# Performance work log

Hardware: AMD Instinct MI355X
Metric: run time of the kernel (lower is better)

Reference implementation:

```python
import jax, jax.numpy as jnp
import numpy as np
import math

WP, WF = 10, 10      # past/future window
EPS = 1e-8           # torch cosine_similarity eps
CLIP = 1.0 - 1e-6    # keep arccos (and its grad) finite
MAXN = 110           # hard-coded alpha width in the module


def setup_inputs() -> dict:
    key = jax.random.key(0)
    k1, k2, k3, k4, k5, k6 = jax.random.split(key, 6)
    B, L, G, N, D = 32, 110, 512, 40, 300
    node_features = jax.random.normal(k1, (B, L, G), jnp.float32)
    knowledge = jax.random.normal(k2, (B, L, N, D), jnp.float32)
    anew = jax.random.uniform(k3, (B, L, N), jnp.float32)
    var_sem = 2.0 / (G + G)
    var_con = 2.0 / (D + D)
    weight_sem = jax.random.normal(k4, (G, G), jnp.float32) * var_sem
    weight_con = jax.random.normal(k5, (D, D), jnp.float32) * var_con
    text_len = jax.random.randint(k6, (B,), 55, L + 1, jnp.int32)
    return dict(node_features=node_features, knowledge=knowledge, anew=anew,
                weight_sem=weight_sem, weight_con=weight_con, text_len=text_len)


def reference(node_features, knowledge, anew, weight_sem, weight_con, text_len):
    B, L, G = node_features.shape
    N = knowledge.shape[2]
    dt = node_features.dtype

    # window + validity mask, replaces per-(i,j) python slicing: [B, j, k]
    j = jnp.arange(L)[:, None]
    k = jnp.arange(L)[None, :]
    cur = text_len[:, None, None]
    mask = (k >= j - WP) & (k <= j + WF)
    mask = mask[None] & (k[None, :, :] <= cur - 1) & (j[None, :, :] < cur)
    fmask = mask.astype(dt)

    # ---- semantic branch: score = 1 - acos(cos_sim(f_j, W_sem f_k))/pi, windowed softmax
    att_sem = jnp.einsum('st,blt->bls', weight_sem, node_features)      # [B,L,G]
    num = jnp.einsum('bjg,bkg->bjk', node_features, att_sem)
    nf = jnp.maximum(jnp.linalg.norm(node_features, axis=-1), EPS)      # [B,L]
    na = jnp.maximum(jnp.linalg.norm(att_sem, axis=-1), EPS)            # [B,L]
    cos = num / (nf[:, :, None] * na[:, None, :])
    score = 1.0 - jnp.arccos(jnp.clip(cos, -CLIP, CLIP)) / math.pi
    neg = jnp.finfo(dt).min
    s = jnp.where(mask, score, neg)
    s = s - jnp.max(s, axis=-1, keepdims=True)
    e = jnp.exp(s) * fmask
    alphas_sem = e / jnp.maximum(jnp.sum(e, axis=-1, keepdims=True), EPS)  # [B,L,L]

    # ---- affinity transform of anew: v -> (||[v, v/2] - [0.5, 0]|| - 0.06467)/0.607468
    anew_aff = (jnp.sqrt((anew - 0.5) ** 2 + (0.5 * anew) ** 2) - 0.06467) / 0.607468

    # ---- contextual branch: windowed sum_n |cos_sim(aff_feat_{k,n}, knowledge_{j,n})|
    att_con = jnp.einsum('blns,st->blnt', knowledge, weight_con)        # [B,L,N,D]
    aff_feat = att_con * anew_aff[..., None]                            # [B,L,N,D]
    num_c = jnp.einsum('bknd,bjnd->bjkn', aff_feat, knowledge)          # [B,j,k,N]
    n_f = jnp.maximum(jnp.linalg.norm(aff_feat, axis=-1), EPS)          # [B,k,N]
    n_k = jnp.maximum(jnp.linalg.norm(knowledge, axis=-1), EPS)         # [B,j,N]
    cos_c = num_c / (n_f[:, None, :, :] * n_k[:, :, None, :])
    alphas_con = 10.0 * jnp.sum(jnp.abs(cos_c), axis=-1) * fmask        # [B,j,k]

    out = 0.5 * alphas_sem + 0.5 * alphas_con                           # [B,L,L]
    if L < MAXN:  # module hard-codes width 110
        out = jnp.pad(out, ((0, 0), (0, 0), (0, MAXN - L)))
    return out
```

## Files before the change

### kernel.cpp

```cpp
#include <hip/hip_runtime.h>
#include <hip/hip_bf16.h>
#include <math.h>

constexpr int Bb   = 32;
constexpr int Ls   = 110;
constexpr int Gs   = 512;
constexpr int Ns   = 40;
constexpr int Ds   = 300;
constexpr int WPc  = 10;
constexpr int WFc  = 10;
constexpr int MAXNc = 110;
constexpr float EPSf  = 1e-8f;
constexpr float CLIPf = 1.0f - 1e-6f;
constexpr int BL = Bb * Ls;
constexpr int Mrows = BL * Ns;

typedef __attribute__((ext_vector_type(8))) short short8_t;
typedef __attribute__((ext_vector_type(4))) short short4_t;
typedef __attribute__((ext_vector_type(4))) float floatx4;

__device__ __forceinline__ unsigned short bf16r(float f) {
  unsigned u = __float_as_uint(f);
  u += 0x7fffu + ((u >> 16) & 1u);
  return (unsigned short)(u >> 16);
}

__device__ __forceinline__ unsigned pkbf(float lo, float hi) {
  unsigned a = __float_as_uint(lo), b = __float_as_uint(hi);
  a += 0x7fffu + ((a >> 16) & 1u);
  b += 0x7fffu + ((b >> 16) & 1u);
  return (a >> 16) | (b & 0xffff0000u);
}

__device__ __forceinline__ short8_t cvt8(const float4 v0, const float4 v1) {
  union { short8_t s; unsigned u[4]; } p;
  p.u[0] = pkbf(v0.x, v0.y);
  p.u[1] = pkbf(v0.z, v0.w);
  p.u[2] = pkbf(v1.x, v1.y);
  p.u[3] = pkbf(v1.z, v1.w);
  return p.s;
}

__global__ __launch_bounds__(256) void transpose_wsem(const float* __restrict__ w,
                                                      float* __restrict__ wt) {
  __shared__ float tile[32][33];
  const int bx = blockIdx.x * 32;
  const int by = blockIdx.y * 32;
  const int tx = threadIdx.x;
  const int ty = threadIdx.y;
#pragma unroll
  for (int r = ty; r < 32; r += 8)
    tile[r][tx] = w[(by + r) * Gs + (bx + tx)];
  __syncthreads();
#pragma unroll
  for (int r = ty; r < 32; r += 8)
    wt[(bx + r) * Gs + (by + tx)] = tile[tx][r];
}

__global__ __launch_bounds__(256) void wct_prep(const float* __restrict__ wc,
                                                short* __restrict__ wct) {
  __shared__ float tile[32][33];
  const int t0 = blockIdx.x * 32;
  const int s0 = blockIdx.y * 32;
  const int tx = threadIdx.x, ty = threadIdx.y;
#pragma unroll
  for (int r = ty; r < 32; r += 8) {
    const int s = s0 + r, t = t0 + tx;
    tile[r][tx] = (s < Ds && t < Ds) ? wc[s * Ds + t] : 0.f;
  }
  __syncthreads();
#pragma unroll
  for (int r = ty; r < 32; r += 8) {
    const int t = t0 + r, s = s0 + tx;
    wct[t * 320 + s] = (short)bf16r(tile[tx][r]);
  }
}

__global__ __launch_bounds__(512) void sem_gemm(const float* __restrict__ nf,
                                                const float* __restrict__ wt,
                                                float* __restrict__ att_sem,
                                                float* __restrict__ na_arr) {
  const int bl0 = blockIdx.x * 8;
  const int s = threadIdx.x;
  const float* __restrict__ x0 = nf + (size_t)bl0 * Gs;
  float acc[8];
#pragma unroll
  for (int r = 0; r < 8; ++r) acc[r] = 0.f;
#pragma unroll 4
  for (int t = 0; t < Gs; ++t) {
    const float wv = wt[t * Gs + s];
#pragma unroll
    for (int r = 0; r < 8; ++r) acc[r] = fmaf(wv, x0[r * Gs + t], acc[r]);
  }
#pragma unroll
  for (int r = 0; r < 8; ++r) att_sem[(size_t)(bl0 + r) * Gs + s] = acc[r];

  __shared__ float partial[8][8];
  const int wave = s >> 6, lane = s & 63;
#pragma unroll
  for (int r = 0; r < 8; ++r) {
    float v = acc[r] * acc[r];
#pragma unroll
    for (int off = 32; off > 0; off >>= 1) v += __shfl_xor(v, off);
    if (lane == 0) partial[r][wave] = v;
  }
  __syncthreads();
  if (s < 8) {
    float sum = 0.f;
#pragma unroll
    for (int w2 = 0; w2 < 8; ++w2) sum += partial[s][w2];
    na_arr[bl0 + s] = fmaxf(sqrtf(sum), EPSf);
  }
}

__global__ __launch_bounds__(256) void sem_attn(const float* __restrict__ nf,
                                                const float* __restrict__ att_sem,
                                                const float* __restrict__ na_arr,
                                                const int* __restrict__ tlen,
                                                float* __restrict__ out) {
  const int blk = blockIdx.x;
  const int b = blk / Ls, j = blk % Ls;
  const int len = tlen[b];
  float* __restrict__ orow = out + (size_t)(b * Ls + j) * MAXNc;
  if (j >= len) {
    for (int k = threadIdx.x; k < MAXNc; k += 256) orow[k] = 0.f;
    return;
  }
  const int k0 = max(j - WPc, 0);
  const int k1 = min(j + WFc, len - 1);
  const int nk = k1 - k0 + 1;

  __shared__ float xs[Gs];
  __shared__ float sc[21];
  __shared__ float red[4];

  const float* __restrict__ x = nf + (size_t)(b * Ls + j) * Gs;
  float ss = 0.f;
  for (int t = threadIdx.x; t < Gs; t += 256) {
    const float v = x[t];
    xs[t] = v;
    ss += v * v;
  }
  const int wave = threadIdx.x >> 6, lane = threadIdx.x & 63;
#pragma unroll
  for (int off = 32; off > 0; off >>= 1) ss += __shfl_xor(ss, off);
  if (lane == 0) red[wave] = ss;
  __syncthreads();
  const float nfn = fmaxf(sqrtf(red[0] + red[1] + red[2] + red[3]), EPSf);

  for (int i = wave; i < nk; i += 4) {
    const int k = k0 + i;
    const float* __restrict__ as = att_sem + (size_t)(b * Ls + k) * Gs;
    float d = 0.f;
#pragma unroll
    for (int t = lane; t < Gs; t += 64) d = fmaf(xs[t], as[t], d);
#pragma unroll
    for (int off = 32; off > 0; off >>= 1) d += __shfl_xor(d, off);
    if (lane == 0) {
      float cs = d / (nfn * na_arr[b * Ls + k]);
      cs = fminf(fmaxf(cs, -CLIPf), CLIPf);
      sc[i] = 1.0f - acosf(cs) * (float)(1.0 / M_PI);
    }
  }
  __syncthreads();
  if (threadIdx.x == 0) {
    float m = -1e30f;
    for (int i = 0; i < nk; ++i) m = fmaxf(m, sc[i]);
    red[0] = m;
  }
  __syncthreads();
  const float m = red[0];
  if ((int)threadIdx.x < nk) sc[threadIdx.x] = expf(sc[threadIdx.x] - m);
  __syncthreads();
  if (threadIdx.x == 0) {
    float s = 0.f;
    for (int i = 0; i < nk; ++i) s += sc[i];
    red[1] = 1.0f / fmaxf(s, EPSf);
  }
  __syncthreads();
  const float inv = red[1];
  for (int k = threadIdx.x; k < MAXNc; k += 256) {
    float v = 0.f;
    if (k >= k0 && k <= k1) v = 0.5f * sc[k - k0] * inv;
    orow[k] = v;
  }
}

__global__ __launch_bounds__(256) void con_gemm_mfma(const float* __restrict__ kn,
                                                     const short* __restrict__ wct,
                                                     const float* __restrict__ anew,
                                                     const int* __restrict__ tlen,
                                                     unsigned short* __restrict__ ybar) {
  const int row0 = blockIdx.x * 64;
  {
    const int bl0 = row0 / Ns, bl1 = (row0 + 63) / Ns;
    bool alive = false;
    for (int bl = bl0; bl <= bl1; ++bl)
      if ((bl % Ls) < tlen[bl / Ls]) alive = true;
    if (!alive) return;
  }

  __shared__ float rowss[64][4];
  __shared__ float scl[64];

  const int tid = threadIdx.x;
  const int wave = tid >> 6, lane = tid & 63;
  const int quad = lane >> 4, l16 = lane & 15;

  floatx4 acc[4][5];
#pragma unroll
  for (int mt = 0; mt < 4; ++mt)
#pragma unroll
    for (int i = 0; i < 5; ++i) acc[mt][i] = (floatx4){0.f, 0.f, 0.f, 0.f};

  const float* arow[4];
#pragma unroll
  for (int mt = 0; mt < 4; ++mt)
    arow[mt] = kn + (size_t)(row0 + mt * 16 + l16) * Ds;

  const short* brow[5];
#pragma unroll
  for (int i = 0; i < 5; ++i)
    brow[i] = wct + (wave * 80 + i * 16 + l16) * 320 + quad * 8;

  for (int c = 0; c < 9; ++c) {
    const int d0 = c * 32 + quad * 8;
    short8_t bfrag[5];
#pragma unroll
    for (int i = 0; i < 5; ++i)
      bfrag[i] = *reinterpret_cast<const short8_t*>(brow[i] + c * 32);
#pragma unroll
    for (int mt = 0; mt < 4; ++mt) {
      const float4 v0 = *reinterpret_cast<const float4*>(arow[mt] + d0);
      const float4 v1 = *reinterpret_cast<const float4*>(arow[mt] + d0 + 4);
      const short8_t afrag = cvt8(v0, v1);
#pragma unroll
      for (int i = 0; i < 5; ++i)
        acc[mt][i] = __builtin_amdgcn_mfma_f32_16x16x32_bf16(afrag, bfrag[i], acc[mt][i], 0, 0, 0);
    }
  }

  {
    const int d0 = 288 + quad * 8;
    short8_t bfrag[5];
#pragma unroll
    for (int i = 0; i < 5; ++i)
      bfrag[i] = *reinterpret_cast<const short8_t*>(brow[i] + 288);
#pragma unroll
    for (int mt = 0; mt < 4; ++mt) {
      float4 v0 = make_float4(0.f, 0.f, 0.f, 0.f);
      float4 v1 = make_float4(0.f, 0.f, 0.f, 0.f);
      if (quad == 0) {
        v0 = *reinterpret_cast<const float4*>(arow[mt] + d0);
        v1 = *reinterpret_cast<const float4*>(arow[mt] + d0 + 4);
      } else if (quad == 1) {
        v0 = *reinterpret_cast<const float4*>(arow[mt] + d0);
      }
      const short8_t afrag = cvt8(v0, v1);
#pragma unroll
      for (int i = 0; i < 5; ++i)
        acc[mt][i] = __builtin_amdgcn_mfma_f32_16x16x32_bf16(afrag, bfrag[i], acc[mt][i], 0, 0, 0);
    }
  }

#pragma unroll
  for (int mt = 0; mt < 4; ++mt) {
#pragma unroll
    for (int r = 0; r < 4; ++r) {
      float p = 0.f;
#pragma unroll
      for (int i = 0; i < 5; ++i) {
        const float y = acc[mt][i][r];
        p = fmaf(y, y, p);
      }
      p += __shfl_xor(p, 1);
      p += __shfl_xor(p, 2);
      p += __shfl_xor(p, 4);
      p += __shfl_xor(p, 8);
      if (l16 == 0) rowss[mt * 16 + quad * 4 + r][wave] = p;
    }
  }
  __syncthreads();
  if (tid < 64) {
    const float ss = rowss[tid][0] + rowss[tid][1] + rowss[tid][2] + rowss[tid][3];
    const float a = anew[row0 + tid];
    const float aff = (sqrtf((a - 0.5f) * (a - 0.5f) + 0.25f * a * a) - 0.06467f) *
                      (1.0f / 0.607468f);
    scl[tid] = aff / fmaxf(aff * sqrtf(ss), EPSf);
  }
  __syncthreads();

#pragma unroll
  for (int mt = 0; mt < 4; ++mt) {
#pragma unroll
    for (int i = 0; i < 5; ++i) {
      const int col = wave * 80 + i * 16 + l16;
      if (col < Ds) {
#pragma unroll
        for (int r = 0; r < 4; ++r) {
          const int row = mt * 16 + quad * 4 + r;
          ybar[(size_t)(row0 + row) * Ds + col] = bf16r(acc[mt][i][r] * scl[row]);
        }
      }
    }
  }
}

__global__ __launch_bounds__(512) void con_attn_mfma(const float* __restrict__ kn,
                                                     const unsigned short* __restrict__ ybar,
                                                     const int* __restrict__ tlen,
                                                     float* __restrict__ out) {
  const int b = blockIdx.x / 7;
  const int jt = blockIdx.x % 7;
  const int j0 = jt * 16;
  const int len = tlen[b];
  if (j0 >= len) return;
  const int kbase = min(max(j0 - WPc, 0), Ls - 48);

  const int tid = threadIdx.x;
  const int wave = tid >> 6, lane = tid & 63;
  const int quad = lane >> 4, l16 = lane & 15;

  __shared__ float red[8][768];

  const int jj = min(j0 + l16, Ls - 1);
  const size_t blj = (size_t)(b * Ls + jj);

  float outacc[3][4];
#pragma unroll
  for (int t = 0; t < 3; ++t)
#pragma unroll
    for (int r = 0; r < 4; ++r) outacc[t][r] = 0.f;

  const unsigned short* yrow[3];
#pragma unroll
  for (int t = 0; t < 3; ++t) {
    const int k = kbase + t * 16 + l16;
    yrow[t] = ybar + ((size_t)(b * Ls + k) * Ns) * Ds;
  }

  for (int ni = 0; ni < 5; ++ni) {
    const int n = wave + ni * 8;
    const float* __restrict__ arow = kn + (blj * Ns + n) * Ds;

    floatx4 S[3];
#pragma unroll
    for (int t = 0; t < 3; ++t) S[t] = (floatx4){0.f, 0.f, 0.f, 0.f};
    float ssq = 0.f;

#pragma unroll
    for (int c = 0; c < 10; ++c) {
      const int d0 = c * 32 + quad * 8;
      float av[8];
      if (c < 9) {
        const float4 v0 = *reinterpret_cast<const float4*>(arow + d0);
        const float4 v1 = *reinterpret_cast<const float4*>(arow + d0 + 4);
        av[0] = v0.x; av[1] = v0.y; av[2] = v0.z; av[3] = v0.w;
        av[4] = v1.x; av[5] = v1.y; av[6] = v1.z; av[7] = v1.w;
      } else {
        if (quad == 0) {
          const float4 v0 = *reinterpret_cast<const float4*>(arow + d0);
          const float4 v1 = *reinterpret_cast<const float4*>(arow + d0 + 4);
          av[0] = v0.x; av[1] = v0.y; av[2] = v0.z; av[3] = v0.w;
          av[4] = v1.x; av[5] = v1.y; av[6] = v1.z; av[7] = v1.w;
        } else if (quad == 1) {
          const float4 v0 = *reinterpret_cast<const float4*>(arow + d0);
          av[0] = v0.x; av[1] = v0.y; av[2] = v0.z; av[3] = v0.w;
          av[4] = av[5] = av[6] = av[7] = 0.f;
        } else {
#pragma unroll
          for (int e = 0; e < 8; ++e) av[e] = 0.f;
        }
      }
      short8_t afrag;
#pragma unroll
      for (int e = 0; e < 8; ++e) {
        ssq = fmaf(av[e], av[e], ssq);
        afrag[e] = (short)bf16r(av[e]);
      }
#pragma unroll
      for (int t = 0; t < 3; ++t) {
        const unsigned short* yr = yrow[t] + (size_t)n * Ds;
        short8_t bfrag;
        if (c < 9) {
          const short4_t u0 = *reinterpret_cast<const short4_t*>(yr + d0);
          const short4_t u1 = *reinterpret_cast<const short4_t*>(yr + d0 + 4);
          bfrag[0] = u0.x; bfrag[1] = u0.y; bfrag[2] = u0.z; bfrag[3] = u0.w;
          bfrag[4] = u1.x; bfrag[5] = u1.y; bfrag[6] = u1.z; bfrag[7] = u1.w;
        } else {
          if (quad == 0) {
            const short4_t u0 = *reinterpret_cast<const short4_t*>(yr + d0);
            const short4_t u1 = *reinterpret_cast<const short4_t*>(yr + d0 + 4);
            bfrag[0] = u0.x; bfrag[1] = u0.y; bfrag[2] = u0.z; bfrag[3] = u0.w;
            bfrag[4] = u1.x; bfrag[5] = u1.y; bfrag[6] = u1.z; bfrag[7] = u1.w;
          } else if (quad == 1) {
            const short4_t u0 = *reinterpret_cast<const short4_t*>(yr + d0);
            bfrag[0] = u0.x; bfrag[1] = u0.y; bfrag[2] = u0.z; bfrag[3] = u0.w;
            bfrag[4] = bfrag[5] = bfrag[6] = bfrag[7] = 0;
          } else {
#pragma unroll
            for (int e = 0; e < 8; ++e) bfrag[e] = 0;
          }
        }
        S[t] = __builtin_amdgcn_mfma_f32_16x16x32_bf16(afrag, bfrag, S[t], 0, 0, 0);
      }
    }

    ssq += __shfl_xor(ssq, 16);
    ssq += __shfl_xor(ssq, 32);
    const float kinv = 1.0f / fmaxf(sqrtf(ssq), EPSf);

#pragma unroll
    for (int r = 0; r < 4; ++r) {
      const float kv = __shfl(kinv, quad * 4 + r);
#pragma unroll
      for (int t = 0; t < 3; ++t)
        outacc[t][r] = fmaf(kv, fabsf(S[t][r]), outacc[t][r]);
    }
  }

#pragma unroll
  for (int t = 0; t < 3; ++t)
#pragma unroll
    for (int r = 0; r < 4; ++r)
      red[wave][(quad * 4 + r) * 48 + t * 16 + l16] = outacc[t][r];
  __syncthreads();

  for (int idx = tid; idx < 768; idx += 512) {
    float s = 0.f;
#pragma unroll
    for (int w = 0; w < 8; ++w) s += red[w][idx];
    const int j = j0 + idx / 48;
    const int k = kbase + idx % 48;
    if (j < len && k < len && k >= j - WPc && k <= j + WFc)
      out[(size_t)(b * Ls + j) * MAXNc + k] += 5.0f * s;
  }
}

extern "C" void kernel_launch(void* const* d_in, const int* in_sizes, int n_in,
                              void* d_out, int out_size, void* d_ws, size_t ws_size,
                              hipStream_t stream) {
  const float* nf   = (const float*)d_in[0];
  const float* kn   = (const float*)d_in[1];
  const float* anew = (const float*)d_in[2];
  const float* wsem = (const float*)d_in[3];
  const float* wcon = (const float*)d_in[4];
  const int*   tlen = (const int*)d_in[5];
  float* out = (float*)d_out;

  float* att_sem = (float*)d_ws;
  float* na_arr  = att_sem + (size_t)BL * Gs;
  float* wt      = na_arr + BL;
  short* wct     = (short*)(wt + (size_t)Gs * Gs);
  unsigned short* ybar = (unsigned short*)(wct + 320 * 320);

  transpose_wsem<<<dim3(16, 16), dim3(32, 8), 0, stream>>>(wsem, wt);
  wct_prep<<<dim3(10, 10), dim3(32, 8), 0, stream>>>(wcon, wct);
  sem_gemm<<<BL / 8, 512, 0, stream>>>(nf, wt, att_sem, na_arr);
  sem_attn<<<BL, 256, 0, stream>>>(nf, att_sem, na_arr, tlen, out);
  con_gemm_mfma<<<Mrows / 64, 256, 0, stream>>>(kn, wct, anew, tlen, ybar);
  con_attn_mfma<<<Bb * 7, 512, 0, stream>>>(kn, ybar, tlen, out);
}
```

Before: 541.7 us.

## Split contextual GEMM over output columns, stage weights in LDS, defer row scaling

The contextual GEMM now runs on a 2D grid: each block computes 64 rows by 80 output columns, with one 16-row tile per wave. The block's slice of the bf16 weight is staged once in padded shared memory, and the fp32 knowledge rows are prefetched through a rotating 3-deep register pipeline. Row sums of squares are accumulated across column blocks with global atomics into a memset buffer, so ybar is stored unscaled. The attention kernel then applies the anew affinity scaling and norm per (k,n) itself. The aim is more parallelism and lower register pressure. The cost is that each A row is read four times, plus atomics, an extra memset, and extra per-iteration loads in the attention kernel.

Result: faster. 513.2 us (-5.2%).

```diff
diff --git a/kernel.cpp b/kernel.cpp
--- a/kernel.cpp
+++ b/kernel.cpp
@@ -14,6 +14,7 @@
 constexpr float CLIPf = 1.0f - 1e-6f;
 constexpr int BL = Bb * Ls;
 constexpr int Mrows = BL * Ns;
+constexpr int BPITCH = 328;
 
 typedef __attribute__((ext_vector_type(8))) short short8_t;
 typedef __attribute__((ext_vector_type(4))) short short4_t;
@@ -188,9 +189,9 @@
 
 __global__ __launch_bounds__(256) void con_gemm_mfma(const float* __restrict__ kn,
                                                      const short* __restrict__ wct,
-                                                     const float* __restrict__ anew,
                                                      const int* __restrict__ tlen,
-                                                     unsigned short* __restrict__ ybar) {
+                                                     unsigned short* __restrict__ ybar,
+                                                     float* __restrict__ rowss) {
   const int row0 = blockIdx.x * 64;
   {
     const int bl0 = row0 / Ns, bl1 = (row0 + 63) / Ns;
@@ -199,108 +200,89 @@
       if ((bl % Ls) < tlen[bl / Ls]) alive = true;
     if (!alive) return;
   }
-
-  __shared__ float rowss[64][4];
-  __shared__ float scl[64];
+  const int n0 = blockIdx.y * 80;
+
+  __shared__ short Bl[80 * BPITCH];
 
   const int tid = threadIdx.x;
   const int wave = tid >> 6, lane = tid & 63;
   const int quad = lane >> 4, l16 = lane & 15;
 
-  floatx4 acc[4][5];
-#pragma unroll
-  for (int mt = 0; mt < 4; ++mt)
-#pragma unroll
-    for (int i = 0; i < 5; ++i) acc[mt][i] = (floatx4){0.f, 0.f, 0.f, 0.f};
-
-  const float* arow[4];
-#pragma unroll
-  for (int mt = 0; mt < 4; ++mt)
-    arow[mt] = kn + (size_t)(row0 + mt * 16 + l16) * Ds;
-
-  const short* brow[5];
-#pragma unroll
-  for (int i = 0; i < 5; ++i)
-    brow[i] = wct + (wave * 80 + i * 16 + l16) * 320 + quad * 8;
-
-  for (int c = 0; c < 9; ++c) {
-    const int d0 = c * 32 + quad * 8;
-    short8_t bfrag[5];
-#pragma unroll
-    for (int i = 0; i < 5; ++i)
-      bfrag[i] = *reinterpret_cast<const short8_t*>(brow[i] + c * 32);
-#pragma unroll
-    for (int mt = 0; mt < 4; ++mt) {
-      const float4 v0 = *reinterpret_cast<const float4*>(arow[mt] + d0);
-      const float4 v1 = *reinterpret_cast<const float4*>(arow[mt] + d0 + 4);
-      const short8_t afrag = cvt8(v0, v1);
-#pragma unroll
-      for (int i = 0; i < 5; ++i)
-        acc[mt][i] = __builtin_amdgcn_mfma_f32_16x16x32_bf16(afrag, bfrag[i], acc[mt][i], 0, 0, 0);
-    }
-  }
-
-  {
-    const int d0 = 288 + quad * 8;
-    short8_t bfrag[5];
-#pragma unroll
-    for (int i = 0; i < 5; ++i)
-      bfrag[i] = *reinterpret_cast<const short8_t*>(brow[i] + 288);
-#pragma unroll
-    for (int mt = 0; mt < 4; ++mt) {
-      float4 v0 = make_float4(0.f, 0.f, 0.f, 0.f);
-      float4 v1 = make_float4(0.f, 0.f, 0.f, 0.f);
-      if (quad == 0) {
-        v0 = *reinterpret_cast<const float4*>(arow[mt] + d0);
-        v1 = *reinterpret_cast<const float4*>(arow[mt] + d0 + 4);
-      } else if (quad == 1) {
-        v0 = *reinterpret_cast<const float4*>(arow[mt] + d0);
+  for (int s = tid; s < 80 * 40; s += 256) {
+    const int nl = s / 40, slot = s % 40;
+    *reinterpret_cast<short8_t*>(&Bl[nl * BPITCH + slot * 8]) =
+        *reinterpret_cast<const short8_t*>(wct + (n0 + nl) * 320 + slot * 8);
+  }
+
+  const float* __restrict__ arow = kn + (size_t)(row0 + wave * 16 + l16) * Ds;
+
+  floatx4 acc[5];
+#pragma unroll
+  for (int i = 0; i < 5; ++i) acc[i] = (floatx4){0.f, 0.f, 0.f, 0.f};
+
+  float4 A0[3], A1[3];
+#pragma unroll
+  for (int p = 0; p < 2; ++p) {
+    const int d0 = p * 32 + quad * 8;
+    A0[p] = *reinterpret_cast<const float4*>(arow + d0);
+    A1[p] = *reinterpret_cast<const float4*>(arow + d0 + 4);
+  }
+  __syncthreads();
+
+#pragma unroll
+  for (int c = 0; c < 10; ++c) {
+    if (c < 8) {
+      const int pc = c + 2;
+      const int d0 = pc * 32 + quad * 8;
+      if (pc < 9) {
+        A0[pc % 3] = *reinterpret_cast<const float4*>(arow + d0);
+        A1[pc % 3] = *reinterpret_cast<const float4*>(arow + d0 + 4);
+      } else {
+        float4 v0 = make_float4(0.f, 0.f, 0.f, 0.f);
+        float4 v1 = make_float4(0.f, 0.f, 0.f, 0.f);
+        if (quad == 0) {
+          v0 = *reinterpret_cast<const float4*>(arow + d0);
+          v1 = *reinterpret_cast<const float4*>(arow + d0 + 4);
+        } else if (quad == 1) {
+          v0 = *reinterpret_cast<const float4*>(arow + d0);
+        }
+        A0[pc % 3] = v0;
+        A1[pc % 3] = v1;
       }
-      const short8_t afrag = cvt8(v0, v1);
-#pragma unroll
-      for (int i = 0; i < 5; ++i)
-        acc[mt][i] = __builtin_amdgcn_mfma_f32_16x16x32_bf16(afrag, bfrag[i], acc[mt][i], 0, 0, 0);
-    }
-  }
-
-#pragma unroll
-  for (int mt = 0; mt < 4; ++mt) {
-#pragma unroll
-    for (int r = 0; r < 4; ++r) {
-      float p = 0.f;
-#pragma unroll
-      for (int i = 0; i < 5; ++i) {
-        const float y = acc[mt][i][r];
-        p = fmaf(y, y, p);
-      }
-      p += __shfl_xor(p, 1);
-      p += __shfl_xor(p, 2);
-      p += __shfl_xor(p, 4);
-      p += __shfl_xor(p, 8);
-      if (l16 == 0) rowss[mt * 16 + quad * 4 + r][wave] = p;
-    }
-  }
-  __syncthreads();
-  if (tid < 64) {
-    const float ss = rowss[tid][0] + rowss[tid][1] + rowss[tid][2] + rowss[tid][3];
-    const float a = anew[row0 + tid];
-    const float aff = (sqrtf((a - 0.5f) * (a - 0.5f) + 0.25f * a * a) - 0.06467f) *
-                      (1.0f / 0.607468f);
-    scl[tid] = aff / fmaxf(aff * sqrtf(ss), EPSf);
-  }
-  __syncthreads();
-
-#pragma unroll
-  for (int mt = 0; mt < 4; ++mt) {
+    }
+    const short8_t afrag = cvt8(A0[c % 3], A1[c % 3]);
 #pragma unroll
     for (int i = 0; i < 5; ++i) {
-      const int col = wave * 80 + i * 16 + l16;
-      if (col < Ds) {
-#pragma unroll
-        for (int r = 0; r < 4; ++r) {
-          const int row = mt * 16 + quad * 4 + r;
-          ybar[(size_t)(row0 + row) * Ds + col] = bf16r(acc[mt][i][r] * scl[row]);
-        }
+      const short8_t bfrag = *reinterpret_cast<const short8_t*>(
+          &Bl[(i * 16 + l16) * BPITCH + c * 32 + quad * 8]);
+      acc[i] = __builtin_amdgcn_mfma_f32_16x16x32_bf16(afrag, bfrag, acc[i], 0, 0, 0);
+    }
+  }
+
+#pragma unroll
+  for (int r = 0; r < 4; ++r) {
+    float p = 0.f;
+#pragma unroll
+    for (int i = 0; i < 5; ++i) {
+      const float y = acc[i][r];
+      p = fmaf(y, y, p);
+    }
+    p += __shfl_xor(p, 1);
+    p += __shfl_xor(p, 2);
+    p += __shfl_xor(p, 4);
+    p += __shfl_xor(p, 8);
+    if (l16 == 0)
+      atomicAdd(&rowss[row0 + wave * 16 + quad * 4 + r], p);
+  }
+
+#pragma unroll
+  for (int i = 0; i < 5; ++i) {
+    const int col = n0 + i * 16 + l16;
+    if (col < Ds) {
+#pragma unroll
+      for (int r = 0; r < 4; ++r) {
+        const int row = row0 + wave * 16 + quad * 4 + r;
+        ybar[(size_t)row * Ds + col] = bf16r(acc[i][r]);
       }
     }
   }
@@ -308,6 +290,8 @@
 
 __global__ __launch_bounds__(512) void con_attn_mfma(const float* __restrict__ kn,
                                                      const unsigned short* __restrict__ ybar,
+                                                     const float* __restrict__ rowss,
+                                                     const float* __restrict__ anew,
                                                      const int* __restrict__ tlen,
                                                      float* __restrict__ out) {
   const int b = blockIdx.x / 7;
@@ -333,15 +317,28 @@
     for (int r = 0; r < 4; ++r) outacc[t][r] = 0.f;
 
   const unsigned short* yrow[3];
+  int krow_m[3];
 #pragma unroll
   for (int t = 0; t < 3; ++t) {
     const int k = kbase + t * 16 + l16;
     yrow[t] = ybar + ((size_t)(b * Ls + k) * Ns) * Ds;
+    krow_m[t] = (b * Ls + k) * Ns;
   }
 
   for (int ni = 0; ni < 5; ++ni) {
     const int n = wave + ni * 8;
     const float* __restrict__ arow = kn + (blj * Ns + n) * Ds;
+
+    float w_t[3];
+#pragma unroll
+    for (int t = 0; t < 3; ++t) {
+      const int m = krow_m[t] + n;
+      const float a = anew[m];
+      const float ssqk = rowss[m];
+      const float aff = (sqrtf((a - 0.5f) * (a - 0.5f) + 0.25f * a * a) - 0.06467f) *
+                        (1.0f / 0.607468f);
+      w_t[t] = aff / fmaxf(aff * sqrtf(ssqk), EPSf);
+    }
 
     floatx4 S[3];
 #pragma unroll
@@ -415,7 +412,7 @@
       const float kv = __shfl(kinv, quad * 4 + r);
 #pragma unroll
       for (int t = 0; t < 3; ++t)
-        outacc[t][r] = fmaf(kv, fabsf(S[t][r]), outacc[t][r]);
+        outacc[t][r] = fmaf(kv * w_t[t], fabsf(S[t][r]), outacc[t][r]);
     }
   }
 
@@ -452,12 +449,14 @@
   float* na_arr  = att_sem + (size_t)BL * Gs;
   float* wt      = na_arr + BL;
   short* wct     = (short*)(wt + (size_t)Gs * Gs);
-  unsigned short* ybar = (unsigned short*)(wct + 320 * 320);
-
+  float* rowss   = (float*)(wct + 320 * 320);
+  unsigned short* ybar = (unsigned short*)(rowss + Mrows);
+
+  hipMemsetAsync(rowss, 0, (size_t)Mrows * sizeof(float), stream);
   transpose_wsem<<<dim3(16, 16), dim3(32, 8), 0, stream>>>(wsem, wt);
   wct_prep<<<dim3(10, 10), dim3(32, 8), 0, stream>>>(wcon, wct);
   sem_gemm<<<BL / 8, 512, 0, stream>>>(nf, wt, att_sem, na_arr);
   sem_attn<<<BL, 256, 0, stream>>>(nf, att_sem, na_arr, tlen, out);
-  con_gemm_mfma<<<Mrows / 64, 256, 0, stream>>>(kn, wct, anew, tlen, ybar);
-  con_attn_mfma<<<Bb * 7, 512, 0, stream>>>(kn, ybar, tlen, out);
-}
+  con_gemm_mfma<<<dim3(Mrows / 64, 4), 256, 0, stream>>>(kn, wct, tlen, ybar, rowss);
+  con_attn_mfma<<<Bb * 7, 512, 0, stream>>>(kn, ybar, rowss, anew, tlen, out);
+}
```
